# Performance work log

Measured on AMD Instinct MI355X. Metric: run time of the kernel, lower is better.

## Reference

```python
import jax, jax.numpy as jnp
import numpy as np


def setup_inputs() -> dict:
    key = jax.random.key(0)
    kx, ky = jax.random.split(key)
    x = jax.random.normal(kx, (4096, 256), dtype=jnp.float32)
    y = jax.random.normal(ky, (16384, 256), dtype=jnp.float32)
    return {"x": x, "y": y}


def reference(x, y):
    # Original module: scan over rows of x; for each row x_i compute
    #   sqrt(sum((y - x_i)**2, axis=1))  -> stacked to [Nx, Ny].
    # Batched equivalent (single fused pass, no serial scan):
    #   ||x_i - y_j||^2 = ||x_i||^2 + ||y_j||^2 - 2 <x_i, y_j>
    x2 = jnp.sum(x * x, axis=1)                       # [Nx]
    y2 = jnp.sum(y * y, axis=1)                       # [Ny]
    xy = jnp.einsum("nd,md->nm", x, y)               # [Nx, Ny]
    d2 = x2[:, None] + y2[None, :] - 2.0 * xy
    return jnp.sqrt(jnp.maximum(d2, 0.0))            # [Nx, Ny]
```

## Files before the change

### kernel.cpp

```cpp
#include <hip/hip_runtime.h>
#include <hip/hip_bf16.h>


using bf16x8  = __attribute__((ext_vector_type(8))) short;
using f32x4   = __attribute__((ext_vector_type(4))) float;
using ushort8 = __attribute__((ext_vector_type(8))) unsigned short;

constexpr int NXR = 4096;
constexpr int NYR = 16384;
constexpr int DD  = 256;

constexpr int BM = 128;
constexpr int BN = 128;
constexpr int BK = 128;
constexpr int PK = BK + 8;

__device__ inline unsigned short f2bf(float f) {
    unsigned int b = __float_as_uint(f);
    b += 0x7FFFu + ((b >> 16) & 1u);
    return (unsigned short)(b >> 16);
}

__global__ __launch_bounds__(256) void norms_kernel(const float* __restrict__ x,
                                                    const float* __restrict__ y,
                                                    float* __restrict__ ws) {
    const int row  = blockIdx.x * 4 + (threadIdx.x >> 6);
    const int lane = threadIdx.x & 63;
    const float* src = (row < NXR) ? (x + (size_t)row * DD)
                                   : (y + (size_t)(row - NXR) * DD);
    float4 v = *(const float4*)(src + lane * 4);
    float s = v.x * v.x + v.y * v.y + v.z * v.z + v.w * v.w;
    #pragma unroll
    for (int off = 32; off > 0; off >>= 1) s += __shfl_down(s, off, 64);
    if (lane == 0) ws[row] = s;
}

__global__ __launch_bounds__(512) void dist_kernel(const float* __restrict__ x,
                                                   const float* __restrict__ y,
                                                   const float* __restrict__ xn,
                                                   const float* __restrict__ yn,
                                                   float* __restrict__ out) {
    __shared__ unsigned short lA[BM * PK];
    __shared__ unsigned short lB[BN * PK];

    const int bm = blockIdx.x;
    const int bn = blockIdx.y;
    const int tid  = threadIdx.x;
    const int wave = tid >> 6;
    const int lane = tid & 63;
    const int wm   = wave & 1;
    const int wn   = wave >> 1;
    const int quad = lane >> 4;
    const int l15  = lane & 15;

    f32x4 acc[4][2];
    #pragma unroll
    for (int i = 0; i < 4; ++i)
        #pragma unroll
        for (int j = 0; j < 2; ++j)
            acc[i][j] = f32x4{0.f, 0.f, 0.f, 0.f};

    const int sc  = (tid & 15) * 8;
    const int sr0 = tid >> 4;

    #pragma unroll
    for (int kt = 0; kt < 2; ++kt) {
        if (kt) __syncthreads();
        #pragma unroll
        for (int p = 0; p < 4; ++p) {
            const int r = p * 32 + sr0;
            const float* sa = x + (size_t)(bm * BM + r) * DD + kt * BK + sc;
            float4 a0 = *(const float4*)sa;
            float4 a1 = *(const float4*)(sa + 4);
            ushort8 ua = { f2bf(a0.x), f2bf(a0.y), f2bf(a0.z), f2bf(a0.w),
                           f2bf(a1.x), f2bf(a1.y), f2bf(a1.z), f2bf(a1.w) };
            *(ushort8*)&lA[r * PK + sc] = ua;
            const float* sb = y + (size_t)(bn * BN + r) * DD + kt * BK + sc;
            float4 b0 = *(const float4*)sb;
            float4 b1 = *(const float4*)(sb + 4);
            ushort8 ub = { f2bf(b0.x), f2bf(b0.y), f2bf(b0.z), f2bf(b0.w),
                           f2bf(b1.x), f2bf(b1.y), f2bf(b1.z), f2bf(b1.w) };
            *(ushort8*)&lB[r * PK + sc] = ub;
        }
        __syncthreads();
        const int ar = (wm * 64 + l15) * PK;
        const int br = (wn * 32 + l15) * PK;
        #pragma unroll
        for (int kk = 0; kk < 4; ++kk) {
            const int k = kk * 32 + quad * 8;
            bf16x8 av[4], bv[2];
            #pragma unroll
            for (int i = 0; i < 4; ++i)
                av[i] = *(const bf16x8*)&lA[ar + i * 16 * PK + k];
            #pragma unroll
            for (int j = 0; j < 2; ++j)
                bv[j] = *(const bf16x8*)&lB[br + j * 16 * PK + k];
            #pragma unroll
            for (int i = 0; i < 4; ++i)
                #pragma unroll
                for (int j = 0; j < 2; ++j)
                    acc[i][j] = __builtin_amdgcn_mfma_f32_16x16x32_bf16(
                        av[i], bv[j], acc[i][j], 0, 0, 0);
        }
    }

    const int gr_base = bm * BM + wm * 64;
    const int gc_base = bn * BN + wn * 32;
    #pragma unroll
    for (int i = 0; i < 4; ++i) {
        const int gr0 = gr_base + i * 16 + quad * 4;
        #pragma unroll
        for (int r = 0; r < 4; ++r) {
            const float xv = xn[gr0 + r];
            const size_t ro = (size_t)(gr0 + r) * NYR;
            #pragma unroll
            for (int j = 0; j < 2; ++j) {
                const int gc = gc_base + j * 16 + l15;
                const float d2 = xv + yn[gc] - 2.0f * acc[i][j][r];
                out[ro + gc] = sqrtf(fmaxf(d2, 0.0f));
            }
        }
    }
}

extern "C" void kernel_launch(void* const* d_in, const int* in_sizes, int n_in,
                              void* d_out, int out_size, void* d_ws, size_t ws_size,
                              hipStream_t stream) {
    const float* x = (const float*)d_in[0];
    const float* y = (const float*)d_in[1];
    float* ws  = (float*)d_ws;
    float* out = (float*)d_out;

    norms_kernel<<<(NXR + NYR) / 4, 256, 0, stream>>>(x, y, ws);
    dist_kernel<<<dim3(NXR / BM, NYR / BN), 512, 0, stream>>>(x, y, ws, ws + NXR, out);
}
```

Baseline: 335.1 us.

## Pre-convert inputs to bf16, load via global_load_lds with XOR swizzle, vectorize stores

Measured after the change: 335.3 us. No clear change (+0.1%).

```diff
diff --git a/kernel.cpp b/kernel.cpp
--- a/kernel.cpp
+++ b/kernel.cpp
@@ -2,18 +2,15 @@
 #include <hip/hip_bf16.h>
 
 
-using bf16x8  = __attribute__((ext_vector_type(8))) short;
-using f32x4   = __attribute__((ext_vector_type(4))) float;
-using ushort8 = __attribute__((ext_vector_type(8))) unsigned short;
+using bf16x8 = __attribute__((ext_vector_type(8))) short;
+using f32x4  = __attribute__((ext_vector_type(4))) float;
 
 constexpr int NXR = 4096;
 constexpr int NYR = 16384;
 constexpr int DD  = 256;
 
-constexpr int BM = 128;
-constexpr int BN = 128;
+constexpr int BT = 128;
 constexpr int BK = 128;
-constexpr int PK = BK + 8;
 
 __device__ inline unsigned short f2bf(float f) {
     unsigned int b = __float_as_uint(f);
@@ -21,37 +18,48 @@
     return (unsigned short)(b >> 16);
 }
 
-__global__ __launch_bounds__(256) void norms_kernel(const float* __restrict__ x,
-                                                    const float* __restrict__ y,
-                                                    float* __restrict__ ws) {
+#define GLDS(gp, lp) __builtin_amdgcn_global_load_lds(                      \
+    (const __attribute__((address_space(1))) void*)(gp),                    \
+    (__attribute__((address_space(3))) void*)(lp), 16, 0, 0)
+
+__global__ __launch_bounds__(256) void prep_kernel(const float* __restrict__ x,
+                                                   const float* __restrict__ y,
+                                                   unsigned short* __restrict__ xb,
+                                                   unsigned short* __restrict__ yb,
+                                                   float* __restrict__ xn,
+                                                   float* __restrict__ yn) {
     const int row  = blockIdx.x * 4 + (threadIdx.x >> 6);
     const int lane = threadIdx.x & 63;
-    const float* src = (row < NXR) ? (x + (size_t)row * DD)
-                                   : (y + (size_t)(row - NXR) * DD);
+    const bool isx = row < NXR;
+    const int r    = isx ? row : row - NXR;
+    const float* src = (isx ? x : y) + (size_t)r * DD;
     float4 v = *(const float4*)(src + lane * 4);
+    ushort4 u = { f2bf(v.x), f2bf(v.y), f2bf(v.z), f2bf(v.w) };
+    unsigned short* dst = (isx ? xb : yb) + (size_t)r * DD;
+    *(ushort4*)(dst + lane * 4) = u;
     float s = v.x * v.x + v.y * v.y + v.z * v.z + v.w * v.w;
     #pragma unroll
     for (int off = 32; off > 0; off >>= 1) s += __shfl_down(s, off, 64);
-    if (lane == 0) ws[row] = s;
+    if (lane == 0) { if (isx) xn[r] = s; else yn[r] = s; }
 }
 
-__global__ __launch_bounds__(512) void dist_kernel(const float* __restrict__ x,
-                                                   const float* __restrict__ y,
+__global__ __launch_bounds__(512) void dist_kernel(const unsigned short* __restrict__ xb,
+                                                   const unsigned short* __restrict__ yb,
                                                    const float* __restrict__ xn,
                                                    const float* __restrict__ yn,
                                                    float* __restrict__ out) {
-    __shared__ unsigned short lA[BM * PK];
-    __shared__ unsigned short lB[BN * PK];
+    __shared__ unsigned short lY[BT * BK];
+    __shared__ unsigned short lX[BT * BK];
 
     const int bm = blockIdx.x;
     const int bn = blockIdx.y;
     const int tid  = threadIdx.x;
     const int wave = tid >> 6;
     const int lane = tid & 63;
+    const int quad = lane >> 4;
+    const int l15  = lane & 15;
     const int wm   = wave & 1;
     const int wn   = wave >> 1;
-    const int quad = lane >> 4;
-    const int l15  = lane & 15;
 
     f32x4 acc[4][2];
     #pragma unroll
@@ -60,41 +68,34 @@
         for (int j = 0; j < 2; ++j)
             acc[i][j] = f32x4{0.f, 0.f, 0.f, 0.f};
 
-    const int sc  = (tid & 15) * 8;
-    const int sr0 = tid >> 4;
+    const int srow_in_wave = lane >> 4;
+    const int sslot        = lane & 15;
 
     #pragma unroll
     for (int kt = 0; kt < 2; ++kt) {
         if (kt) __syncthreads();
         #pragma unroll
         for (int p = 0; p < 4; ++p) {
-            const int r = p * 32 + sr0;
-            const float* sa = x + (size_t)(bm * BM + r) * DD + kt * BK + sc;
-            float4 a0 = *(const float4*)sa;
-            float4 a1 = *(const float4*)(sa + 4);
-            ushort8 ua = { f2bf(a0.x), f2bf(a0.y), f2bf(a0.z), f2bf(a0.w),
-                           f2bf(a1.x), f2bf(a1.y), f2bf(a1.z), f2bf(a1.w) };
-            *(ushort8*)&lA[r * PK + sc] = ua;
-            const float* sb = y + (size_t)(bn * BN + r) * DD + kt * BK + sc;
-            float4 b0 = *(const float4*)sb;
-            float4 b1 = *(const float4*)(sb + 4);
-            ushort8 ub = { f2bf(b0.x), f2bf(b0.y), f2bf(b0.z), f2bf(b0.w),
-                           f2bf(b1.x), f2bf(b1.y), f2bf(b1.z), f2bf(b1.w) };
-            *(ushort8*)&lB[r * PK + sc] = ub;
+            const int r = p * 32 + wave * 4 + srow_in_wave;
+            const int c = sslot ^ (r & 15);
+            const size_t goff = (size_t)r * DD + kt * BK + c * 8;
+            GLDS(yb + (size_t)(bn * BT) * DD + goff, &lY[(p * 8 + wave) * 512]);
+            GLDS(xb + (size_t)(bm * BT) * DD + goff, &lX[(p * 8 + wave) * 512]);
         }
         __syncthreads();
-        const int ar = (wm * 64 + l15) * PK;
-        const int br = (wn * 32 + l15) * PK;
+
+        const int ybase = (wm * 64 + l15) * BK;
+        const int xbase = (wn * 32 + l15) * BK;
         #pragma unroll
         for (int kk = 0; kk < 4; ++kk) {
-            const int k = kk * 32 + quad * 8;
+            const int sw = ((kk * 4 + quad) ^ l15) * 8;
             bf16x8 av[4], bv[2];
             #pragma unroll
             for (int i = 0; i < 4; ++i)
-                av[i] = *(const bf16x8*)&lA[ar + i * 16 * PK + k];
+                av[i] = *(const bf16x8*)&lY[ybase + i * 16 * BK + sw];
             #pragma unroll
             for (int j = 0; j < 2; ++j)
-                bv[j] = *(const bf16x8*)&lB[br + j * 16 * PK + k];
+                bv[j] = *(const bf16x8*)&lX[xbase + j * 16 * BK + sw];
             #pragma unroll
             for (int i = 0; i < 4; ++i)
                 #pragma unroll
@@ -104,21 +105,21 @@
         }
     }
 
-    const int gr_base = bm * BM + wm * 64;
-    const int gc_base = bn * BN + wn * 32;
+    const int xr0 = bm * BT + wn * 32;
+    const int yc0 = bn * BT + wm * 64;
     #pragma unroll
     for (int i = 0; i < 4; ++i) {
-        const int gr0 = gr_base + i * 16 + quad * 4;
+        const int ycol = yc0 + i * 16 + quad * 4;
+        const f32x4 ynv = *(const f32x4*)&yn[ycol];
         #pragma unroll
-        for (int r = 0; r < 4; ++r) {
-            const float xv = xn[gr0 + r];
-            const size_t ro = (size_t)(gr0 + r) * NYR;
+        for (int j = 0; j < 2; ++j) {
+            const int xrow = xr0 + j * 16 + l15;
+            const float xv = xn[xrow];
+            f32x4 d;
             #pragma unroll
-            for (int j = 0; j < 2; ++j) {
-                const int gc = gc_base + j * 16 + l15;
-                const float d2 = xv + yn[gc] - 2.0f * acc[i][j][r];
-                out[ro + gc] = sqrtf(fmaxf(d2, 0.0f));
-            }
+            for (int r = 0; r < 4; ++r)
+                d[r] = sqrtf(fmaxf(xv + ynv[r] - 2.0f * acc[i][j][r], 0.0f));
+            *(f32x4*)&out[(size_t)xrow * NYR + ycol] = d;
         }
     }
 }
@@ -128,9 +129,13 @@
                               hipStream_t stream) {
     const float* x = (const float*)d_in[0];
     const float* y = (const float*)d_in[1];
-    float* ws  = (float*)d_ws;
     float* out = (float*)d_out;
 
-    norms_kernel<<<(NXR + NYR) / 4, 256, 0, stream>>>(x, y, ws);
-    dist_kernel<<<dim3(NXR / BM, NYR / BN), 512, 0, stream>>>(x, y, ws, ws + NXR, out);
+    unsigned short* xb = (unsigned short*)d_ws;
+    unsigned short* yb = xb + (size_t)NXR * DD;
+    float* xn = (float*)(yb + (size_t)NYR * DD);
+    float* yn = xn + NXR;
+
+    prep_kernel<<<(NXR + NYR) / 4, 256, 0, stream>>>(x, y, xb, yb, xn, yn);
+    dist_kernel<<<dim3(NXR / BT, NYR / BT), 512, 0, stream>>>(xb, yb, xn, yn, out);
 }
```
